# Kernel tuning notes

Hardware: AMD Instinct MI355X
Metric: run time of the kernel (lower is better)

## Reference

```python
import jax, jax.numpy as jnp
import numpy as np

# 6 ordered (src, tgt) pairs among 3 modalities, in the same nested-loop order as torch
SRC = jnp.array([0, 0, 1, 1, 2, 2])
TGT = jnp.array([1, 2, 0, 2, 0, 1])

B, L, H, G = 16384, 256, 96, 32
P = 6  # number of translation directions


def _layernorm(x, gamma, beta, eps=1e-5):
    # x: [P, B, F]; gamma/beta: [P, 1, F]
    m = jnp.mean(x, axis=-1, keepdims=True)
    v = jnp.mean((x - m) ** 2, axis=-1, keepdims=True)
    return (x - m) * jax.lax.rsqrt(v + eps) * gamma + beta


def setup_inputs() -> dict:
    key = jax.random.key(0)
    ks = jax.random.split(key, 20)
    f32 = jnp.float32
    d = {}
    d['mus'] = jax.random.normal(ks[0], (3, B, L), f32)
    d['logvars'] = jax.random.normal(ks[1], (3, B, L), f32)
    d['mask'] = jax.random.randint(ks[2], (B, 3), 0, 2).astype(bool)
    # translation head params (stacked over the 6 pairs)
    d['hw1'] = jax.random.normal(ks[3], (P, 2 * L, H), f32) / np.sqrt(2 * L)
    d['hb1'] = jax.random.normal(ks[4], (P, H), f32) * 0.02
    d['hg1'] = jnp.ones((P, H), f32)
    d['hbe1'] = jnp.zeros((P, H), f32)
    d['hw2'] = jax.random.normal(ks[5], (P, H, H), f32) / np.sqrt(H)
    d['hb2'] = jax.random.normal(ks[6], (P, H), f32) * 0.02
    d['hg2'] = jnp.ones((P, H), f32)
    d['hbe2'] = jnp.zeros((P, H), f32)
    d['hw3'] = jax.random.normal(ks[7], (P, H, 2 * L), f32) / np.sqrt(H)
    d['hb3'] = jax.random.normal(ks[8], (P, 2 * L), f32) * 0.02
    # gate network params
    d['gw1'] = jax.random.normal(ks[9], (P, 2 * L, G), f32) / np.sqrt(2 * L)
    d['gb1'] = jax.random.normal(ks[10], (P, G), f32) * 0.02
    d['gg1'] = jnp.ones((P, G), f32)
    d['gbe1'] = jnp.zeros((P, G), f32)
    d['gw2'] = jax.random.normal(ks[11], (P, G, 1), f32) / np.sqrt(G)
    d['gb2'] = jnp.full((P, 1), -1.0, f32)
    return d


def reference(mus, logvars, mask, hw1, hb1, hg1, hbe1, hw2, hb2, hg2, hbe2,
              hw3, hb3, gw1, gb1, gg1, gbe1, gw2, gb2):
    latent = mus.shape[-1]
    # gather source posteriors per pair and concat: [P, B, 2L]
    h = jnp.concatenate([mus[SRC], logvars[SRC]], axis=-1)
    # translation head: Linear -> LN -> GELU (x2) -> Linear
    x = jax.nn.gelu(_layernorm(jnp.einsum('pbi,pih->pbh', h, hw1) + hb1[:, None, :],
                               hg1[:, None, :], hbe1[:, None, :]), approximate=False)
    x = jax.nn.gelu(_layernorm(jnp.einsum('pbh,phk->pbk', x, hw2) + hb2[:, None, :],
                               hg2[:, None, :], hbe2[:, None, :]), approximate=False)
    out = jnp.einsum('pbh,pho->pbo', x, hw3) + hb3[:, None, :]  # [P, B, 2L]
    mu_pseudo = out[..., :latent]
    lv_pseudo = jnp.clip(out[..., latent:], -6.0, 2.0)
    # gate: Linear -> LN -> GELU -> Linear -> sigmoid
    g = jax.nn.gelu(_layernorm(jnp.einsum('pbi,pig->pbg', h, gw1) + gb1[:, None, :],
                               gg1[:, None, :], gbe1[:, None, :]), approximate=False)
    gate = jax.nn.sigmoid(jnp.einsum('pbg,pgo->pbo', g, gw2) + gb2[:, None, :])  # [P, B, 1]
    # only keep rows where source observed and target missing; others are zero-filled
    needs = (mask[:, SRC] & ~mask[:, TGT]).T  # [P, B]
    m3 = needs[:, :, None]
    zero = jnp.zeros((), mu_pseudo.dtype)
    return (jnp.where(m3, mu_pseudo, zero),
            jnp.where(m3, lv_pseudo, zero),
            jnp.where(m3, gate, zero))
```

## Files before the change

### kernel.cpp

```cpp
#include <hip/hip_runtime.h>
#include <hip/hip_bf16.h>
#include <math.h>

#define B_ 16384
#define NP 6

typedef short v8s __attribute__((ext_vector_type(8)));
typedef short v4s __attribute__((ext_vector_type(4)));
typedef float v4f __attribute__((ext_vector_type(4)));

__device__ __forceinline__ float gelu_f(float x) {
    return 0.5f * x * (1.0f + erff(x * 0.7071067811865476f));
}
__device__ __forceinline__ unsigned short f2bf(float f) {
    union { float f; unsigned u; } x; x.f = f;
    unsigned r = x.u + 0x7FFFu + ((x.u >> 16) & 1u);
    return (unsigned short)(r >> 16);
}
__device__ __forceinline__ short bfs(float f) {
    union { __hip_bfloat16 h; unsigned short u; } cv;
    cv.h = __float2bfloat16(f);
    return (short)cv.u;
}

__global__ __launch_bounds__(256) void k_prep(
    const float* __restrict__ hw1, const float* __restrict__ gw1,
    const float* __restrict__ hw2, const float* __restrict__ hw3,
    unsigned short* __restrict__ w1t, unsigned short* __restrict__ w2f,
    unsigned short* __restrict__ w3f)
{
    const int T1 = NP * 65536, T2 = NP * 9216, T3 = NP * 49152;
    for (int i = blockIdx.x * 256 + threadIdx.x; i < T1 + T2 + T3; i += gridDim.x * 256) {
        if (i < T1) {
            int p = i >> 16, rem = i & 65535, c = rem >> 9, k = rem & 511;
            float v = (c < 96) ? hw1[p * 49152 + k * 96 + c] : gw1[p * 16384 + k * 32 + (c - 96)];
            w1t[i] = f2bf(v);
        } else if (i < T1 + T2) {
            int j2 = i - T1, p = j2 / 9216, rem = j2 % 9216;
            int f = rem >> 9, within = rem & 511;
            int qg = within >> 3, j = within & 7;
            int q = qg >> 2, g = qg & 3;
            int k = (f % 3) * 32 + g * 8 + j;
            int col = (f / 3) * 16 + q;
            w2f[j2] = f2bf(hw2[p * 9216 + k * 96 + col]);
        } else {
            int j3 = i - T1 - T2, p = j3 / 49152, rem = j3 % 49152;
            int f = rem >> 9, within = rem & 511;
            int qg = within >> 3, j = within & 7;
            int q = qg >> 2, g = qg & 3;
            int k = (f % 3) * 32 + g * 8 + j;
            int col = (f / 3) * 16 + q;
            w3f[j3] = f2bf(hw3[p * 49152 + k * 512 + col]);
        }
    }
}

__global__ __launch_bounds__(256) void k_count(
    const int* __restrict__ mask, int* __restrict__ counts, int* __restrict__ lists)
{
    int p   = blockIdx.x >> 3;
    int seg = blockIdx.x & 7;
    int src = p >> 1;
    int tgt = (0x102021 >> (p * 4)) & 0xF;
    int t = threadIdx.x;
    int lane = t & 63;
    for (int it = 0; it < 8; ++it) {
        int b = seg * 2048 + it * 256 + t;
        int needs = (mask[b * 3 + src] != 0) && (mask[b * 3 + tgt] == 0);
        unsigned long long bal = __ballot(needs);
        int total = __popcll(bal);
        int base = 0;
        if (lane == 0 && total) base = atomicAdd(&counts[p], total);
        base = __shfl(base, 0, 64);
        if (needs) {
            int prefix = __popcll(bal & ((1ull << lane) - 1ull));
            lists[p * B_ + base + prefix] = b;
        }
    }
}

__global__ __launch_bounds__(512, 2) void k_main(
    const float* __restrict__ mus, const float* __restrict__ logvars,
    const unsigned short* __restrict__ w1t, const unsigned short* __restrict__ w2f,
    const unsigned short* __restrict__ w3f,
    const float* __restrict__ hb1, const float* __restrict__ hg1, const float* __restrict__ hbe1,
    const float* __restrict__ hb2, const float* __restrict__ hg2, const float* __restrict__ hbe2,
    const float* __restrict__ hb3,
    const float* __restrict__ gb1, const float* __restrict__ gg1, const float* __restrict__ gbe1,
    const float* __restrict__ gw2, const float* __restrict__ gb2,
    const int* __restrict__ counts, const int* __restrict__ lists,
    float* __restrict__ out0, float* __restrict__ out1, float* __restrict__ out2)
{
    int cb = blockIdx.x;
    int p  = cb % 6, blk = cb / 6;
    int t  = threadIdx.x;
    int w  = t >> 6, l = t & 63, g = l >> 4, q = l & 15;
    int cnt = counts[p];

    __shared__ __align__(16) unsigned short smW[128 * 512];
    __shared__ __align__(16) unsigned short smX[8 * 1664];

    const unsigned short* w1p = w1t + (size_t)p * 65536;
    const unsigned short* w2p = w2f + (size_t)p * 9216;
    const unsigned short* w3p = w3f + (size_t)p * 49152;

    int start = (blk * 8 + w) * 16;
    bool active = start < cnt;
    int nr = active ? min(16, cnt - start) : 0;
    int myrow = active ? lists[p * B_ + min(start + q, cnt - 1)] : 0;
    const float* Ab = mus     + (size_t)(p >> 1) * B_ * 256 + (size_t)myrow * 256 + g * 8;
    const float* Lb = logvars + (size_t)(p >> 1) * B_ * 256 + (size_t)myrow * 256 + g * 8;

    float4 ma[8], mb[8];
    if (active) {
#pragma unroll
        for (int k = 0; k < 8; ++k) {
            ma[k] = *(const float4*)(Ab + k * 32);
            mb[k] = *(const float4*)(Ab + k * 32 + 4);
        }
    }

    {
        int c = t >> 2, qt = t & 3;
        const unsigned short* src = w1p + c * 512 + qt * 128;
        unsigned short* dstrow = smW + c * 512;
        int cx = c & 7;
#pragma unroll
        for (int jj = 0; jj < 16; ++jj) {
            int j = qt * 16 + jj;
            *(v8s*)(dstrow + (((j ^ cx)) << 3)) = *(const v8s*)(src + jj * 8);
        }
    }
    __syncthreads();

    unsigned short* mX = smX + w * 1664;
    float gb2p = gb2[p];

    if (active) {
        v4f acc1[8];
#pragma unroll
        for (int n = 0; n < 8; ++n) acc1[n] = (v4f){0.f, 0.f, 0.f, 0.f};

        int qx = q & 7;
        float4 la[8], lb[8];
#pragma unroll
        for (int kt = 0; kt < 8; ++kt) {
            la[kt] = *(const float4*)(Lb + kt * 32);
            lb[kt] = *(const float4*)(Lb + kt * 32 + 4);
            v8s a;
            a[0] = bfs(ma[kt].x); a[1] = bfs(ma[kt].y); a[2] = bfs(ma[kt].z); a[3] = bfs(ma[kt].w);
            a[4] = bfs(mb[kt].x); a[5] = bfs(mb[kt].y); a[6] = bfs(mb[kt].z); a[7] = bfs(mb[kt].w);
#pragma unroll
            for (int n = 0; n < 8; ++n) {
                int i = kt * 4 + g;
                v8s b = *(const v8s*)(smW + (n * 16 + q) * 512 + ((i ^ qx) << 3));
                acc1[n] = __builtin_amdgcn_mfma_f32_16x16x32_bf16(b, a, acc1[n], 0, 0, 0);
            }
        }
#pragma unroll
        for (int kt = 0; kt < 8; ++kt) {
            v8s a;
            a[0] = bfs(la[kt].x); a[1] = bfs(la[kt].y); a[2] = bfs(la[kt].z); a[3] = bfs(la[kt].w);
            a[4] = bfs(lb[kt].x); a[5] = bfs(lb[kt].y); a[6] = bfs(lb[kt].z); a[7] = bfs(lb[kt].w);
#pragma unroll
            for (int n = 0; n < 8; ++n) {
                int i = (kt + 8) * 4 + g;
                v8s b = *(const v8s*)(smW + (n * 16 + q) * 512 + ((i ^ qx) << 3));
                acc1[n] = __builtin_amdgcn_mfma_f32_16x16x32_bf16(b, a, acc1[n], 0, 0, 0);
            }
        }

        {
            float vb[8][4];
#pragma unroll
            for (int n = 0; n < 8; ++n) {
                float4 bb = (n < 6) ? *(const float4*)(hb1 + p * 96 + n * 16 + 4 * g)
                                    : *(const float4*)(gb1 + p * 32 + (n - 6) * 16 + 4 * g);
                vb[n][0] = acc1[n][0] + bb.x; vb[n][1] = acc1[n][1] + bb.y;
                vb[n][2] = acc1[n][2] + bb.z; vb[n][3] = acc1[n][3] + bb.w;
            }
            float hs = 0.f;
#pragma unroll
            for (int n = 0; n < 6; ++n)
#pragma unroll
                for (int j = 0; j < 4; ++j) hs += vb[n][j];
            hs += __shfl_xor(hs, 16, 64); hs += __shfl_xor(hs, 32, 64);
            float mean = hs * (1.f / 96.f);
            float sq = 0.f;
#pragma unroll
            for (int n = 0; n < 6; ++n)
#pragma unroll
                for (int j = 0; j < 4; ++j) { float d = vb[n][j] - mean; sq += d * d; }
            sq += __shfl_xor(sq, 16, 64); sq += __shfl_xor(sq, 32, 64);
            float rs = rsqrtf(sq * (1.f / 96.f) + 1e-5f);
#pragma unroll
            for (int n = 0; n < 6; ++n) {
                float4 ga = *(const float4*)(hg1  + p * 96 + n * 16 + 4 * g);
                float4 be = *(const float4*)(hbe1 + p * 96 + n * 16 + 4 * g);
                v4s xo;
                xo[0] = bfs(gelu_f((vb[n][0] - mean) * rs * ga.x + be.x));
                xo[1] = bfs(gelu_f((vb[n][1] - mean) * rs * ga.y + be.y));
                xo[2] = bfs(gelu_f((vb[n][2] - mean) * rs * ga.z + be.z));
                xo[3] = bfs(gelu_f((vb[n][3] - mean) * rs * ga.w + be.w));
                *(v4s*)(mX + q * 104 + n * 16 + 4 * g) = xo;
            }
            float gs = 0.f;
#pragma unroll
            for (int n = 6; n < 8; ++n)
#pragma unroll
                for (int j = 0; j < 4; ++j) gs += vb[n][j];
            gs += __shfl_xor(gs, 16, 64); gs += __shfl_xor(gs, 32, 64);
            float mg = gs * (1.f / 32.f);
            float gq = 0.f;
#pragma unroll
            for (int n = 6; n < 8; ++n)
#pragma unroll
                for (int j = 0; j < 4; ++j) { float d = vb[n][j] - mg; gq += d * d; }
            gq += __shfl_xor(gq, 16, 64); gq += __shfl_xor(gq, 32, 64);
            float rg = rsqrtf(gq * (1.f / 32.f) + 1e-5f);
            float gv = 0.f;
#pragma unroll
            for (int n = 6; n < 8; ++n) {
                int cg = (n - 6) * 16 + 4 * g;
                float4 ga = *(const float4*)(gg1  + p * 32 + cg);
                float4 be = *(const float4*)(gbe1 + p * 32 + cg);
                float4 w2 = *(const float4*)(gw2  + p * 32 + cg);
                gv += gelu_f((vb[n][0] - mg) * rg * ga.x + be.x) * w2.x;
                gv += gelu_f((vb[n][1] - mg) * rg * ga.y + be.y) * w2.y;
                gv += gelu_f((vb[n][2] - mg) * rg * ga.z + be.z) * w2.z;
                gv += gelu_f((vb[n][3] - mg) * rg * ga.w + be.w) * w2.w;
            }
            gv += __shfl_xor(gv, 16, 64); gv += __shfl_xor(gv, 32, 64);
            if (g == 0 && q < nr)
                out2[p * B_ + myrow] = 1.f / (1.f + expf(-(gv + gb2p)));
        }

        {
            v4f acc2[6];
#pragma unroll
            for (int n = 0; n < 6; ++n) acc2[n] = (v4f){0.f, 0.f, 0.f, 0.f};
            int fo = q * 32 + g * 8;
#pragma unroll
            for (int kit = 0; kit < 3; ++kit) {
                v8s xa = *(const v8s*)(mX + q * 104 + kit * 32 + g * 8);
#pragma unroll
                for (int n = 0; n < 6; ++n) {
                    v8s wb = *(const v8s*)(w2p + (n * 3 + kit) * 512 + fo);
                    acc2[n] = __builtin_amdgcn_mfma_f32_16x16x32_bf16(wb, xa, acc2[n], 0, 0, 0);
                }
            }
            float vc[6][4];
#pragma unroll
            for (int n = 0; n < 6; ++n) {
                float4 bb = *(const float4*)(hb2 + p * 96 + n * 16 + 4 * g);
                vc[n][0] = acc2[n][0] + bb.x; vc[n][1] = acc2[n][1] + bb.y;
                vc[n][2] = acc2[n][2] + bb.z; vc[n][3] = acc2[n][3] + bb.w;
            }
            float hs = 0.f;
#pragma unroll
            for (int n = 0; n < 6; ++n)
#pragma unroll
                for (int j = 0; j < 4; ++j) hs += vc[n][j];
            hs += __shfl_xor(hs, 16, 64); hs += __shfl_xor(hs, 32, 64);
            float mean = hs * (1.f / 96.f);
            float sq = 0.f;
#pragma unroll
            for (int n = 0; n < 6; ++n)
#pragma unroll
                for (int j = 0; j < 4; ++j) { float d = vc[n][j] - mean; sq += d * d; }
            sq += __shfl_xor(sq, 16, 64); sq += __shfl_xor(sq, 32, 64);
            float rs = rsqrtf(sq * (1.f / 96.f) + 1e-5f);
#pragma unroll
            for (int n = 0; n < 6; ++n) {
                float4 ga = *(const float4*)(hg2  + p * 96 + n * 16 + 4 * g);
                float4 be = *(const float4*)(hbe2 + p * 96 + n * 16 + 4 * g);
                v4s xo;
                xo[0] = bfs(gelu_f((vc[n][0] - mean) * rs * ga.x + be.x));
                xo[1] = bfs(gelu_f((vc[n][1] - mean) * rs * ga.y + be.y));
                xo[2] = bfs(gelu_f((vc[n][2] - mean) * rs * ga.z + be.z));
                xo[3] = bfs(gelu_f((vc[n][3] - mean) * rs * ga.w + be.w));
                *(v4s*)(mX + q * 104 + n * 16 + 4 * g) = xo;
            }
        }

        {
            size_t base = ((size_t)(p * B_ + myrow)) * 256;
            int fo = q * 32 + g * 8;
#pragma unroll 1
            for (int pc = 0; pc < 4; ++pc) {
                v4f acc3[8];
#pragma unroll
                for (int n = 0; n < 8; ++n) acc3[n] = (v4f){0.f, 0.f, 0.f, 0.f};
#pragma unroll
                for (int kit = 0; kit < 3; ++kit) {
                    v8s xa = *(const v8s*)(mX + q * 104 + kit * 32 + g * 8);
#pragma unroll
                    for (int n = 0; n < 8; ++n) {
                        v8s wb = *(const v8s*)(w3p + ((pc * 8 + n) * 3 + kit) * 512 + fo);
                        acc3[n] = __builtin_amdgcn_mfma_f32_16x16x32_bf16(wb, xa, acc3[n], 0, 0, 0);
                    }
                }
#pragma unroll
                for (int n = 0; n < 8; ++n) {
                    int c = pc * 128 + n * 16 + 4 * g;
                    float4 bb = *(const float4*)(hb3 + p * 512 + c);
                    if (q < nr) {
                        float o0 = acc3[n][0] + bb.x, o1 = acc3[n][1] + bb.y;
                        float o2 = acc3[n][2] + bb.z, o3 = acc3[n][3] + bb.w;
                        if (pc < 2) {
                            *(float4*)(out0 + base + c) = make_float4(o0, o1, o2, o3);
                        } else {
                            o0 = fminf(fmaxf(o0, -6.f), 2.f); o1 = fminf(fmaxf(o1, -6.f), 2.f);
                            o2 = fminf(fmaxf(o2, -6.f), 2.f); o3 = fminf(fmaxf(o3, -6.f), 2.f);
                            *(float4*)(out1 + base + c - 256) = make_float4(o0, o1, o2, o3);
                        }
                    }
                }
            }
        }
    }
}

extern "C" void kernel_launch(void* const* d_in, const int* in_sizes, int n_in,
                              void* d_out, int out_size, void* d_ws, size_t ws_size,
                              hipStream_t stream)
{
    (void)in_sizes; (void)n_in; (void)ws_size;

    const float* mus     = (const float*)d_in[0];
    const float* logvars = (const float*)d_in[1];
    const int*   mask    = (const int*)d_in[2];
    const float* hw1  = (const float*)d_in[3];
    const float* hb1  = (const float*)d_in[4];
    const float* hg1  = (const float*)d_in[5];
    const float* hbe1 = (const float*)d_in[6];
    const float* hw2  = (const float*)d_in[7];
    const float* hb2  = (const float*)d_in[8];
    const float* hg2  = (const float*)d_in[9];
    const float* hbe2 = (const float*)d_in[10];
    const float* hw3  = (const float*)d_in[11];
    const float* hb3  = (const float*)d_in[12];
    const float* gw1  = (const float*)d_in[13];
    const float* gb1  = (const float*)d_in[14];
    const float* gg1  = (const float*)d_in[15];
    const float* gbe1 = (const float*)d_in[16];
    const float* gw2  = (const float*)d_in[17];
    const float* gb2  = (const float*)d_in[18];

    float* out0 = (float*)d_out;
    float* out1 = out0 + (size_t)NP * B_ * 256;
    float* out2 = out1 + (size_t)NP * B_ * 256;

    int* counts = (int*)d_ws;
    int* lists  = counts + 16;
    unsigned short* w1t = (unsigned short*)(lists + NP * B_);
    unsigned short* w2f = w1t + (size_t)NP * 65536;
    unsigned short* w3f = w2f + (size_t)NP * 9216;

    hipMemsetAsync(d_out, 0, (size_t)out_size * sizeof(float), stream);
    hipMemsetAsync(d_ws, 0, 64, stream);
    k_count<<<dim3(NP * 8), dim3(256), 0, stream>>>(mask, counts, lists);
    k_prep<<<dim3(512), dim3(256), 0, stream>>>(hw1, gw1, hw2, hw3, w1t, w2f, w3f);
    k_main<<<dim3(256), dim3(512), 0, stream>>>(
        mus, logvars, w1t, w2f, w3f,
        hb1, hg1, hbe1, hb2, hg2, hbe2, hb3,
        gb1, gg1, gbe1, gw2, gb2,
        counts, lists, out0, out1, out2);
}
```

Baseline: 105.3 us.

## Zero only unselected output rows in main kernel and merge prep kernels

The full-output memset is replaced by per-row zeroing inside the main kernel. A per-pair bitmask of needed rows, recorded during list building, tells each block which rows to clear, so rows that the MLP later overwrites are no longer written twice. The mask-count and weight-prep kernels are merged into one launch, and blocks with no work skip the shared-memory weight staging. The zeroing adds a serial per-row loop to each warp and depends on the chunk partition covering every row exactly once.

Result: faster. 95.90 us (-8.9%).

```diff
diff --git a/kernel.cpp b/kernel.cpp
--- a/kernel.cpp
+++ b/kernel.cpp
@@ -23,14 +23,41 @@
     return (short)cv.u;
 }
 
-__global__ __launch_bounds__(256) void k_prep(
+__global__ __launch_bounds__(256) void k_pre(
+    const int* __restrict__ mask, int* __restrict__ counts,
+    int* __restrict__ lists, unsigned long long* __restrict__ nb,
     const float* __restrict__ hw1, const float* __restrict__ gw1,
     const float* __restrict__ hw2, const float* __restrict__ hw3,
     unsigned short* __restrict__ w1t, unsigned short* __restrict__ w2f,
     unsigned short* __restrict__ w3f)
 {
+    int t = threadIdx.x;
+    if (blockIdx.x < 48) {
+        int p   = blockIdx.x >> 3;
+        int seg = blockIdx.x & 7;
+        int src = p >> 1;
+        int tgt = (0x102021 >> (p * 4)) & 0xF;
+        int lane = t & 63;
+        for (int it = 0; it < 8; ++it) {
+            int b = seg * 2048 + it * 256 + t;
+            int needs = (mask[b * 3 + src] != 0) && (mask[b * 3 + tgt] == 0);
+            unsigned long long bal = __ballot(needs);
+            int total = __popcll(bal);
+            int base = 0;
+            if (lane == 0) {
+                nb[p * 256 + (b >> 6)] = bal;
+                if (total) base = atomicAdd(&counts[p], total);
+            }
+            base = __shfl(base, 0, 64);
+            if (needs) {
+                int prefix = __popcll(bal & ((1ull << lane) - 1ull));
+                lists[p * B_ + base + prefix] = b;
+            }
+        }
+        return;
+    }
     const int T1 = NP * 65536, T2 = NP * 9216, T3 = NP * 49152;
-    for (int i = blockIdx.x * 256 + threadIdx.x; i < T1 + T2 + T3; i += gridDim.x * 256) {
+    for (int i = (blockIdx.x - 48) * 256 + t; i < T1 + T2 + T3; i += 512 * 256) {
         if (i < T1) {
             int p = i >> 16, rem = i & 65535, c = rem >> 9, k = rem & 511;
             float v = (c < 96) ? hw1[p * 49152 + k * 96 + c] : gw1[p * 16384 + k * 32 + (c - 96)];
@@ -55,30 +82,6 @@
     }
 }
 
-__global__ __launch_bounds__(256) void k_count(
-    const int* __restrict__ mask, int* __restrict__ counts, int* __restrict__ lists)
-{
-    int p   = blockIdx.x >> 3;
-    int seg = blockIdx.x & 7;
-    int src = p >> 1;
-    int tgt = (0x102021 >> (p * 4)) & 0xF;
-    int t = threadIdx.x;
-    int lane = t & 63;
-    for (int it = 0; it < 8; ++it) {
-        int b = seg * 2048 + it * 256 + t;
-        int needs = (mask[b * 3 + src] != 0) && (mask[b * 3 + tgt] == 0);
-        unsigned long long bal = __ballot(needs);
-        int total = __popcll(bal);
-        int base = 0;
-        if (lane == 0 && total) base = atomicAdd(&counts[p], total);
-        base = __shfl(base, 0, 64);
-        if (needs) {
-            int prefix = __popcll(bal & ((1ull << lane) - 1ull));
-            lists[p * B_ + base + prefix] = b;
-        }
-    }
-}
-
 __global__ __launch_bounds__(512, 2) void k_main(
     const float* __restrict__ mus, const float* __restrict__ logvars,
     const unsigned short* __restrict__ w1t, const unsigned short* __restrict__ w2f,
@@ -89,6 +92,7 @@
     const float* __restrict__ gb1, const float* __restrict__ gg1, const float* __restrict__ gbe1,
     const float* __restrict__ gw2, const float* __restrict__ gb2,
     const int* __restrict__ counts, const int* __restrict__ lists,
+    const unsigned long long* __restrict__ nb,
     float* __restrict__ out0, float* __restrict__ out1, float* __restrict__ out2)
 {
     int cb = blockIdx.x;
@@ -100,10 +104,31 @@
     __shared__ __align__(16) unsigned short smW[128 * 512];
     __shared__ __align__(16) unsigned short smX[8 * 1664];
 
-    const unsigned short* w1p = w1t + (size_t)p * 65536;
-    const unsigned short* w2p = w2f + (size_t)p * 9216;
-    const unsigned short* w3p = w3f + (size_t)p * 49152;
-
+    {
+        int chunk = (p < 4) ? 384 : 392;
+        int pwr   = chunk >> 3;
+        int zr0   = blk * chunk + w * pwr;
+        int zend  = min(blk * chunk + chunk, B_);
+        int zn    = min(zr0 + pwr, zend) - zr0;
+        if (zn > 0) {
+            int wi0 = zr0 >> 6, wiN = (zr0 + zn - 1) >> 6;
+            unsigned long long w0 = nb[p * 256 + wi0];
+            unsigned long long w1 = nb[p * 256 + wiN];
+            float4 z = make_float4(0.f, 0.f, 0.f, 0.f);
+            for (int i = 0; i < zn; ++i) {
+                int zr = zr0 + i;
+                unsigned long long wd = ((zr >> 6) == wi0) ? w0 : w1;
+                if (!((wd >> (zr & 63)) & 1ull)) {
+                    size_t rb = ((size_t)p * B_ + zr) * 256 + l * 4;
+                    *(float4*)(out0 + rb) = z;
+                    *(float4*)(out1 + rb) = z;
+                    if (l == 0) out2[p * B_ + zr] = 0.f;
+                }
+            }
+        }
+    }
+
+    bool anyStage = (blk * 128) < cnt;
     int start = (blk * 8 + w) * 16;
     bool active = start < cnt;
     int nr = active ? min(16, cnt - start) : 0;
@@ -111,6 +136,10 @@
     const float* Ab = mus     + (size_t)(p >> 1) * B_ * 256 + (size_t)myrow * 256 + g * 8;
     const float* Lb = logvars + (size_t)(p >> 1) * B_ * 256 + (size_t)myrow * 256 + g * 8;
 
+    const unsigned short* w1p = w1t + (size_t)p * 65536;
+    const unsigned short* w2p = w2f + (size_t)p * 9216;
+    const unsigned short* w3p = w3f + (size_t)p * 49152;
+
     float4 ma[8], mb[8];
     if (active) {
 #pragma unroll
@@ -120,18 +149,20 @@
         }
     }
 
-    {
-        int c = t >> 2, qt = t & 3;
-        const unsigned short* src = w1p + c * 512 + qt * 128;
-        unsigned short* dstrow = smW + c * 512;
-        int cx = c & 7;
-#pragma unroll
-        for (int jj = 0; jj < 16; ++jj) {
-            int j = qt * 16 + jj;
-            *(v8s*)(dstrow + (((j ^ cx)) << 3)) = *(const v8s*)(src + jj * 8);
-        }
-    }
-    __syncthreads();
+    if (anyStage) {
+        {
+            int c = t >> 2, qt = t & 3;
+            const unsigned short* src = w1p + c * 512 + qt * 128;
+            unsigned short* dstrow = smW + c * 512;
+            int cx = c & 7;
+#pragma unroll
+            for (int jj = 0; jj < 16; ++jj) {
+                int j = qt * 16 + jj;
+                *(v8s*)(dstrow + (((j ^ cx)) << 3)) = *(const v8s*)(src + jj * 8);
+            }
+        }
+        __syncthreads();
+    }
 
     unsigned short* mX = smX + w * 1664;
     float gb2p = gb2[p];
@@ -325,7 +356,7 @@
                               void* d_out, int out_size, void* d_ws, size_t ws_size,
                               hipStream_t stream)
 {
-    (void)in_sizes; (void)n_in; (void)ws_size;
+    (void)in_sizes; (void)n_in; (void)out_size; (void)ws_size;
 
     const float* mus     = (const float*)d_in[0];
     const float* logvars = (const float*)d_in[1];
@@ -356,14 +387,14 @@
     unsigned short* w1t = (unsigned short*)(lists + NP * B_);
     unsigned short* w2f = w1t + (size_t)NP * 65536;
     unsigned short* w3f = w2f + (size_t)NP * 9216;
-
-    hipMemsetAsync(d_out, 0, (size_t)out_size * sizeof(float), stream);
+    unsigned long long* nbm = (unsigned long long*)(w3f + (size_t)NP * 49152);
+
     hipMemsetAsync(d_ws, 0, 64, stream);
-    k_count<<<dim3(NP * 8), dim3(256), 0, stream>>>(mask, counts, lists);
-    k_prep<<<dim3(512), dim3(256), 0, stream>>>(hw1, gw1, hw2, hw3, w1t, w2f, w3f);
+    k_pre<<<dim3(560), dim3(256), 0, stream>>>(
+        mask, counts, lists, nbm, hw1, gw1, hw2, hw3, w1t, w2f, w3f);
     k_main<<<dim3(256), dim3(512), 0, stream>>>(
         mus, logvars, w1t, w2f, w3f,
         hb1, hg1, hbe1, hb2, hg2, hbe2, hb3,
         gb1, gg1, gbe1, gw2, gb2,
-        counts, lists, out0, out1, out2);
-}
+        counts, lists, nbm, out0, out1, out2);
+}
```
